# Kernel tuning notes

Measured on AMD Instinct MI355X. Metric: run time of the kernel, lower is better.

Reference implementation:

```python
import jax, jax.numpy as jnp
import numpy as np

BETA = 0.25
TEMP = 1.0
K = 1024          # codebook_size
DIM = 256         # dim == z_dim


def setup_inputs() -> dict:
    key = jax.random.key(0)
    k1, k2, k3 = jax.random.split(key, 3)
    x = jax.random.normal(k1, (8, 4096, DIM), dtype=jnp.float32)
    # Linear: kaiming_uniform -> sqrt(3/fan_in) * U(-1,1); bias init_bias=0 -> zeros
    W = np.sqrt(3.0 / DIM) * (jax.random.uniform(k2, (DIM, DIM), dtype=jnp.float32) * 2 - 1)
    b = jnp.zeros((DIM,), dtype=jnp.float32)
    # embedding: uniform(-1/K, 1/K)
    emb = jax.random.uniform(k3, (K, DIM), dtype=jnp.float32,
                             minval=-1.0 / K, maxval=1.0 / K)
    return {"x": x, "W": W, "b": b, "emb": emb}


def reference(x, W, b, emb):
    # proj_in: x @ W.T + b
    z = jnp.einsum('bld,od->blo', x, W) + b                     # [B, L, D]
    # squared-L2 distances to codebook (use_norm=False branch)
    dist = (jnp.sum(z * z, axis=-1, keepdims=True)
            + jnp.sum(emb * emb, axis=1)
            - 2.0 * jnp.einsum('bld,nd->bln', z, emb))           # [B, L, K]
    indices = jnp.argmin(dist, axis=-1)                          # [B, L] int
    # ste_prob computed in torch forward (affects grads via one_hot, not outputs)
    quant = emb[indices]                                         # [B, L, D]
    # commitment + codebook loss (training=True)
    loss = (BETA * jnp.mean((jax.lax.stop_gradient(quant) - z) ** 2)
            + jnp.mean((quant - jax.lax.stop_gradient(z)) ** 2))
    # straight-through estimator
    quant = z + jax.lax.stop_gradient(quant - z)
    return quant, indices, loss
```

## Files before the change

### kernel.cpp

```cpp
#include <hip/hip_runtime.h>
#include <hip/hip_bf16.h>

#define TT 32768
#define DD 256
#define KK 1024
#define B_S 5e-4f

typedef __attribute__((ext_vector_type(8)))  short bf16x8;
typedef __attribute__((ext_vector_type(4)))  short bf16x4s;
typedef __attribute__((ext_vector_type(16))) float f32x16;

static inline __device__ short f2bf(float v) {
    __hip_bfloat16 h = __float2bfloat16(v);
    return __builtin_bit_cast(short, h);
}
static inline __device__ float bf2f(short s) {
    __hip_bfloat16 h = __builtin_bit_cast(__hip_bfloat16, s);
    return __bfloat162float(h);
}

__global__ void k_ee(const float* __restrict__ emb, float* __restrict__ ee,
                     int* __restrict__ g_nf) {
    if (blockIdx.x == 0 && threadIdx.x == 0) g_nf[0] = 0;
    int n = blockIdx.x * 256 + threadIdx.x;
    if (n >= KK) return;
    const float4* r = (const float4*)(emb + (size_t)n * DD);
    float s = 0.f;
#pragma unroll
    for (int i = 0; i < DD / 4; ++i) {
        float4 v = r[i];
        s += v.x * v.x + v.y * v.y + v.z * v.z + v.w * v.w;
    }
    ee[n] = s;
}

__global__ void k_pack(const float* __restrict__ emb, short* __restrict__ pemb,
                       float4* __restrict__ embP4) {
    int u = blockIdx.x * 256 + threadIdx.x;
    int lane = u & 63;
    int ks  = (u >> 6) & 1, nb = (u >> 7) & 3;
    int kbi = (u >> 9) & 7, nc = (u >> 12) & 7;
    int n = nc * 128 + nb * 32 + (lane & 31);
    int k = kbi * 32 + ks * 16 + (lane >> 5) * 8;
    const float* src = emb + (size_t)n * DD + k;
    float4 v0 = *(const float4*)(src);
    float4 v1 = *(const float4*)(src + 4);
    bf16x8 hb = { f2bf(v0.x), f2bf(v0.y), f2bf(v0.z), f2bf(v0.w),
                  f2bf(v1.x), f2bf(v1.y), f2bf(v1.z), f2bf(v1.w) };
    *(bf16x8*)(pemb + (size_t)u * 8) = hb;
    embP4[(size_t)(k >> 2) * KK + n]       = v0;
    embP4[(size_t)((k >> 2) + 1) * KK + n] = v1;
}

#define PW 40

__launch_bounds__(256, 2)
__global__ void k_proj(const float* __restrict__ x, const float* __restrict__ W,
                       const float* __restrict__ bias, float* __restrict__ z) {
    __shared__ __align__(16) short Ax[3][64 * PW];
    __shared__ __align__(16) short Bw[3][256 * PW];
    const int tid = threadIdx.x;
    const int w = tid >> 6, lane = tid & 63;
    const int l31 = lane & 31, h = lane >> 5;
    const int t0 = blockIdx.x * 64;
    const int wt = (w & 1) * 32;
    const int wc = (w >> 1) * 128;

    f32x16 acc[4];
#pragma unroll
    for (int cb = 0; cb < 4; ++cb)
#pragma unroll
        for (int r = 0; r < 16; ++r) acc[cb][r] = 0.f;

    for (int kb = 0; kb < DD; kb += 32) {
        __syncthreads();
#pragma unroll
        for (int j = 0; j < 2; ++j) {
            int idx = j * 256 + tid, row = idx >> 3, c4 = idx & 7;
            float4 v = *(const float4*)(x + (size_t)(t0 + row) * DD + kb + c4 * 4);
            float e[4] = {v.x, v.y, v.z, v.w};
            bf16x4s s1, s2, s3;
#pragma unroll
            for (int q = 0; q < 4; ++q) {
                short h1 = f2bf(e[q]); float r1 = e[q] - bf2f(h1);
                short h2 = f2bf(r1);   float r2 = r1 - bf2f(h2);
                short h3 = f2bf(r2);
                s1[q] = h1; s2[q] = h2; s3[q] = h3;
            }
            int a = row * PW + c4 * 4;
            *(bf16x4s*)&Ax[0][a] = s1; *(bf16x4s*)&Ax[1][a] = s2; *(bf16x4s*)&Ax[2][a] = s3;
        }
#pragma unroll
        for (int j = 0; j < 8; ++j) {
            int idx = j * 256 + tid, row = idx >> 3, c4 = idx & 7;
            float4 v = *(const float4*)(W + (size_t)row * DD + kb + c4 * 4);
            float e[4] = {v.x, v.y, v.z, v.w};
            bf16x4s s1, s2, s3;
#pragma unroll
            for (int q = 0; q < 4; ++q) {
                short h1 = f2bf(e[q]); float r1 = e[q] - bf2f(h1);
                short h2 = f2bf(r1);   float r2 = r1 - bf2f(h2);
                short h3 = f2bf(r2);
                s1[q] = h1; s2[q] = h2; s3[q] = h3;
            }
            int a = row * PW + c4 * 4;
            *(bf16x4s*)&Bw[0][a] = s1; *(bf16x4s*)&Bw[1][a] = s2; *(bf16x4s*)&Bw[2][a] = s3;
        }
        __syncthreads();
#pragma unroll
        for (int ks = 0; ks < 2; ++ks) {
            int ao = (wt + l31) * PW + ks * 16 + h * 8;
            bf16x8 a1 = *(bf16x8*)&Ax[0][ao];
            bf16x8 a2 = *(bf16x8*)&Ax[1][ao];
            bf16x8 a3 = *(bf16x8*)&Ax[2][ao];
#pragma unroll
            for (int cb = 0; cb < 4; ++cb) {
                int bo = (wc + cb * 32 + l31) * PW + ks * 16 + h * 8;
                bf16x8 b1 = *(bf16x8*)&Bw[0][bo];
                bf16x8 b2 = *(bf16x8*)&Bw[1][bo];
                bf16x8 b3 = *(bf16x8*)&Bw[2][bo];
                acc[cb] = __builtin_amdgcn_mfma_f32_32x32x16_bf16(a1, b3, acc[cb], 0, 0, 0);
                acc[cb] = __builtin_amdgcn_mfma_f32_32x32x16_bf16(a2, b2, acc[cb], 0, 0, 0);
                acc[cb] = __builtin_amdgcn_mfma_f32_32x32x16_bf16(a3, b1, acc[cb], 0, 0, 0);
                acc[cb] = __builtin_amdgcn_mfma_f32_32x32x16_bf16(a1, b2, acc[cb], 0, 0, 0);
                acc[cb] = __builtin_amdgcn_mfma_f32_32x32x16_bf16(a2, b1, acc[cb], 0, 0, 0);
                acc[cb] = __builtin_amdgcn_mfma_f32_32x32x16_bf16(a1, b1, acc[cb], 0, 0, 0);
            }
        }
    }
#pragma unroll
    for (int cb = 0; cb < 4; ++cb) {
        int col = wc + cb * 32 + l31;
        float bc = bias[col];
#pragma unroll
        for (int r = 0; r < 16; ++r) {
            int row = (r & 3) + 8 * (r >> 2) + 4 * h;
            z[(size_t)(t0 + wt + row) * DD + col] = acc[cb][r] + bc;
        }
    }
}

#define SW 264

__launch_bounds__(256, 2)
__global__ void k_screen(const float* __restrict__ z, const short* __restrict__ pemb,
                         const float* __restrict__ ee_g, float* __restrict__ out_idx) {
    __shared__ __align__(16) short A_s[64 * SW];
    __shared__ float ee_s[1024];
    __shared__ float zzs[64];
    __shared__ float r_bv[64]; __shared__ int r_bi[64]; __shared__ float r_sv[64];

    const int tid = threadIdx.x;
    const int w = tid >> 6, lane = tid & 63;
    const int l31 = lane & 31, h = lane >> 5;
    const int t0 = blockIdx.x * 64;
    const int wr = (w >> 1) * 32, wc = (w & 1) * 64;

#pragma unroll
    for (int i = 0; i < 4; ++i) ee_s[i * 256 + tid] = ee_g[i * 256 + tid];

#pragma unroll
    for (int i = 0; i < 16; ++i) {
        int tl = i * 4 + w;
        float4 v = *(const float4*)(z + (size_t)(t0 + tl) * DD + lane * 4);
        float sq = v.x * v.x + v.y * v.y + v.z * v.z + v.w * v.w;
#pragma unroll
        for (int o = 32; o; o >>= 1) sq += __shfl_xor(sq, o);
        if (lane == 0) zzs[tl] = sq;
        bf16x4s hb = {f2bf(v.x), f2bf(v.y), f2bf(v.z), f2bf(v.w)};
        *(bf16x4s*)&A_s[tl * SW + lane * 4] = hb;
    }
    __syncthreads();

    const int u00 = ((((w & 1) * 2 + 0) * 2 + 0) * 64 + lane) * 8;
    const int u01 = ((((w & 1) * 2 + 0) * 2 + 1) * 64 + lane) * 8;
    const int u10 = ((((w & 1) * 2 + 1) * 2 + 0) * 64 + lane) * 8;
    const int u11 = ((((w & 1) * 2 + 1) * 2 + 1) * 64 + lane) * 8;

    bf16x8 B00[4], B01[4], B10[4], B11[4];
#pragma unroll
    for (int s = 0; s < 4; ++s) {
        const short* gt = pemb + (size_t)s * 4096;
        B00[s] = *(const bf16x8*)(gt + u00);
        B01[s] = *(const bf16x8*)(gt + u01);
        B10[s] = *(const bf16x8*)(gt + u10);
        B11[s] = *(const bf16x8*)(gt + u11);
    }

    float bestv[16], secv[16]; int besti[16];
#pragma unroll
    for (int r = 0; r < 16; ++r) { bestv[r] = 1e30f; secv[r] = 1e30f; besti[r] = 0; }

    f32x16 acc0, acc1;
    for (int tq = 0; tq < 16; ++tq) {
#pragma unroll
        for (int s = 0; s < 4; ++s) {
            const int t = tq * 4 + s;
            const int nc = t >> 3, kbi = t & 7;
            if (kbi == 0) {
#pragma unroll
                for (int r = 0; r < 16; ++r) { acc0[r] = 0.f; acc1[r] = 0.f; }
            }
            bf16x8 a0 = *(bf16x8*)&A_s[(wr + l31) * SW + kbi * 32 + 0 * 16 + h * 8];
            bf16x8 a1 = *(bf16x8*)&A_s[(wr + l31) * SW + kbi * 32 + 1 * 16 + h * 8];
            acc0 = __builtin_amdgcn_mfma_f32_32x32x16_bf16(a0, B00[s], acc0, 0, 0, 0);
            acc1 = __builtin_amdgcn_mfma_f32_32x32x16_bf16(a0, B10[s], acc1, 0, 0, 0);
            acc0 = __builtin_amdgcn_mfma_f32_32x32x16_bf16(a1, B01[s], acc0, 0, 0, 0);
            acc1 = __builtin_amdgcn_mfma_f32_32x32x16_bf16(a1, B11[s], acc1, 0, 0, 0);
            {
                const int tn = (t + 4 > 63) ? 63 : t + 4;
                const short* gt = pemb + (size_t)tn * 4096;
                B00[s] = *(const bf16x8*)(gt + u00);
                B01[s] = *(const bf16x8*)(gt + u01);
                B10[s] = *(const bf16x8*)(gt + u10);
                B11[s] = *(const bf16x8*)(gt + u11);
            }
            if (kbi == 7) {
#pragma unroll
                for (int j = 0; j < 2; ++j) {
                    int n = nc * 128 + wc + j * 32 + l31;
                    float en = ee_s[n];
#pragma unroll
                    for (int r = 0; r < 16; ++r) {
                        int row = (r & 3) + 8 * (r >> 2) + 4 * h;
                        float u = zzs[wr + row] + en;
                        float d = (j == 0) ? acc0[r] : acc1[r];
                        float sc = fmaf(-2.f, d, u);
                        if (sc < bestv[r])      { secv[r] = bestv[r]; bestv[r] = sc; besti[r] = n; }
                        else if (sc < secv[r])  { secv[r] = sc; }
                    }
                }
            }
        }
    }

#pragma unroll
    for (int o = 1; o < 32; o <<= 1) {
#pragma unroll
        for (int r = 0; r < 16; ++r) {
            float ov = __shfl_xor(bestv[r], o);
            int   oi = __shfl_xor(besti[r], o);
            float os = __shfl_xor(secv[r], o);
            float mx = fmaxf(bestv[r], ov);
            secv[r] = fminf(fminf(secv[r], os), mx);
            if (ov < bestv[r] || (ov == bestv[r] && oi < besti[r])) { bestv[r] = ov; besti[r] = oi; }
        }
    }
    if ((w & 1) == 0 && l31 == 0) {
#pragma unroll
        for (int r = 0; r < 16; ++r) {
            int tr = wr + (r & 3) + 8 * (r >> 2) + 4 * h;
            r_bv[tr] = bestv[r]; r_bi[tr] = besti[r]; r_sv[tr] = secv[r];
        }
    }
    __syncthreads();
    if ((w & 1) == 1 && l31 == 0) {
#pragma unroll
        for (int r = 0; r < 16; ++r) {
            int tr = wr + (r & 3) + 8 * (r >> 2) + 4 * h;
            float lv = r_bv[tr]; int li = r_bi[tr]; float ls = r_sv[tr];
            float mx = fmaxf(lv, bestv[r]);
            float ns = fminf(fminf(ls, secv[r]), mx);
            float nv; int ni;
            if (bestv[r] < lv || (bestv[r] == lv && besti[r] < li)) { nv = bestv[r]; ni = besti[r]; }
            else { nv = lv; ni = li; }
            r_bv[tr] = nv; r_bi[tr] = ni; r_sv[tr] = ns;
        }
    }
    __syncthreads();
    if (tid < 64) {
        float bv = r_bv[tid], sv = r_sv[tid];
        int bi = r_bi[tid];
        float flag = ((sv - bv) < B_S) ? 4096.0f : 0.0f;
        out_idx[t0 + tid] = (float)bi + flag;
    }
}

__global__ void k_compact(const float* __restrict__ out_idx, int* __restrict__ g_nf,
                          int* __restrict__ g_list) {
    __shared__ int wbase[4];
    __shared__ int bbase;
    const int tid = threadIdx.x;
    const int t = blockIdx.x * 256 + tid;
    const int wid = tid >> 6, lane = tid & 63;
    bool fl = out_idx[t] >= 4096.0f;
    unsigned long long m = __ballot(fl);
    if (lane == 0) wbase[wid] = __popcll(m);
    __syncthreads();
    if (tid == 0) {
        int s = 0;
#pragma unroll
        for (int i = 0; i < 4; ++i) { int c = wbase[i]; wbase[i] = s; s += c; }
        bbase = atomicAdd(g_nf, s);
    }
    __syncthreads();
    if (fl) {
        int rank = __popcll(m & ((1ull << lane) - 1ull));
        g_list[bbase + wbase[wid] + rank] = t;
    }
}

#define RB 8

__launch_bounds__(256, 2)
__global__ void k_rescoreT(const float* __restrict__ z, const float4* __restrict__ embP4,
                           const float* __restrict__ ee_g, const int* __restrict__ g_nf,
                           const int* __restrict__ g_list, float* __restrict__ out_idx) {
    __shared__ float zrows[RB][256];
    __shared__ float zz8[RB];
    __shared__ int   toks[RB];
    __shared__ float rv_s[RB][4]; __shared__ int ri_s[RB][4];
    const int tid = threadIdx.x;
    const int w = tid >> 6, lane = tid & 63;
    const int nf = g_nf[0];

    for (int base = blockIdx.x * RB; base < nf; base += gridDim.x * RB) {
        __syncthreads();
        if (tid < RB) toks[tid] = (base + tid < nf) ? g_list[base + tid] : -1;
        __syncthreads();
#pragma unroll
        for (int qq = 0; qq < RB; ++qq) {
            int tok = toks[qq];
            zrows[qq][tid] = (tok >= 0) ? z[(size_t)tok * DD + tid] : 0.f;
        }
        __syncthreads();
        for (int qq = w; qq < RB; qq += 4) {
            float s = 0.f;
#pragma unroll
            for (int k = 0; k < 4; ++k) { float vv = zrows[qq][lane + 64 * k]; s += vv * vv; }
#pragma unroll
            for (int o = 32; o; o >>= 1) s += __shfl_xor(s, o);
            if (lane == 0) zz8[qq] = s;
        }
        __syncthreads();

        float en4[4];
#pragma unroll
        for (int p = 0; p < 4; ++p) en4[p] = ee_g[p * 256 + tid];

        float d[4][RB];
#pragma unroll
        for (int p = 0; p < 4; ++p)
#pragma unroll
            for (int q = 0; q < RB; ++q) d[p][q] = 0.f;

        float4 eA[4], eB[4], zA[RB], zB[RB];
#pragma unroll
        for (int p = 0; p < 4; ++p) eA[p] = embP4[(size_t)0 * KK + p * 256 + tid];
#pragma unroll
        for (int q = 0; q < RB; ++q) zA[q] = *(const float4*)&zrows[q][0];

        for (int k4 = 0; k4 < 64; k4 += 2) {
#pragma unroll
            for (int p = 0; p < 4; ++p) eB[p] = embP4[(size_t)(k4 + 1) * KK + p * 256 + tid];
#pragma unroll
            for (int q = 0; q < RB; ++q) zB[q] = *(const float4*)&zrows[q][(k4 + 1) * 4];
#pragma unroll
            for (int p = 0; p < 4; ++p)
#pragma unroll
                for (int q = 0; q < RB; ++q) {
                    d[p][q] = fmaf(eA[p].x, zA[q].x, d[p][q]);
                    d[p][q] = fmaf(eA[p].y, zA[q].y, d[p][q]);
                    d[p][q] = fmaf(eA[p].z, zA[q].z, d[p][q]);
                    d[p][q] = fmaf(eA[p].w, zA[q].w, d[p][q]);
                }
            if (k4 < 62) {
#pragma unroll
                for (int p = 0; p < 4; ++p) eA[p] = embP4[(size_t)(k4 + 2) * KK + p * 256 + tid];
#pragma unroll
                for (int q = 0; q < RB; ++q) zA[q] = *(const float4*)&zrows[q][(k4 + 2) * 4];
            }
#pragma unroll
            for (int p = 0; p < 4; ++p)
#pragma unroll
                for (int q = 0; q < RB; ++q) {
                    d[p][q] = fmaf(eB[p].x, zB[q].x, d[p][q]);
                    d[p][q] = fmaf(eB[p].y, zB[q].y, d[p][q]);
                    d[p][q] = fmaf(eB[p].z, zB[q].z, d[p][q]);
                    d[p][q] = fmaf(eB[p].w, zB[q].w, d[p][q]);
                }
        }

        float bv[RB]; int bi[RB];
#pragma unroll
        for (int q = 0; q < RB; ++q) { bv[q] = 1e30f; bi[q] = 0; }
#pragma unroll
        for (int p = 0; p < 4; ++p) {
            const int n = p * 256 + tid;
#pragma unroll
            for (int q = 0; q < RB; ++q) {
                float u = zz8[q] + en4[p];
                float s = fmaf(-2.f, d[p][q], u);
                if (s < bv[q]) { bv[q] = s; bi[q] = n; }
            }
        }
        for (int q = 0; q < RB; ++q) {
            float v = bv[q]; int i = bi[q];
#pragma unroll
            for (int o = 1; o < 64; o <<= 1) {
                float ov = __shfl_xor(v, o); int oi = __shfl_xor(i, o);
                if (ov < v || (ov == v && oi < i)) { v = ov; i = oi; }
            }
            if (lane == 0) { rv_s[q][w] = v; ri_s[q][w] = i; }
        }
        __syncthreads();
        if (tid < RB) {
            int tk = toks[tid];
            if (tk >= 0) {
                float fv = rv_s[tid][0]; int fi = ri_s[tid][0];
#pragma unroll
                for (int ww = 1; ww < 4; ++ww) {
                    if (rv_s[tid][ww] < fv || (rv_s[tid][ww] == fv && ri_s[tid][ww] < fi)) {
                        fv = rv_s[tid][ww]; fi = ri_s[tid][ww];
                    }
                }
                out_idx[tk] = (float)fi;
            }
        }
    }
}

__global__ void k_gather(float* __restrict__ zq, const float* __restrict__ emb,
                         const float* __restrict__ out_idx, float* __restrict__ partial) {
    __shared__ float red[4];
    const int tid = threadIdx.x;
    const int t0 = blockIdx.x * 128;
    const int tl = tid >> 1, part = tid & 1;
    int widx = (int)out_idx[t0 + tl];
    widx = min(max(widx, 0), KK - 1);
    const float* erow = emb + (size_t)widx * DD;
    float* qrow = zq + (size_t)(t0 + tl) * DD;
    float lsum = 0.f;
#pragma unroll
    for (int k = 0; k < 32; ++k) {
        int f = part + 2 * k;
        float4 e  = *(const float4*)(erow + f * 4);
        float4 zv = *(const float4*)(qrow + f * 4);
        float dx = e.x - zv.x, dy = e.y - zv.y, dz = e.z - zv.z, dw = e.w - zv.w;
        lsum += dx * dx + dy * dy + dz * dz + dw * dw;
        *(float4*)(qrow + f * 4) = e;
    }
#pragma unroll
    for (int off = 32; off; off >>= 1) lsum += __shfl_down(lsum, off);
    if ((tid & 63) == 0) red[tid >> 6] = lsum;
    __syncthreads();
    if (tid == 0) partial[blockIdx.x] = red[0] + red[1] + red[2] + red[3];
}

__global__ void k_loss(const float* __restrict__ partial, float* __restrict__ out_loss) {
    __shared__ float red[4];
    int tid = threadIdx.x;
    float s = partial[tid];
#pragma unroll
    for (int off = 32; off; off >>= 1) s += __shfl_down(s, off);
    if ((tid & 63) == 0) red[tid >> 6] = s;
    __syncthreads();
    if (tid == 0)
        out_loss[0] = (red[0] + red[1] + red[2] + red[3]) * (1.25f / 8388608.0f);
}

extern "C" void kernel_launch(void* const* d_in, const int* in_sizes, int n_in,
                              void* d_out, int out_size, void* d_ws, size_t ws_size,
                              hipStream_t stream) {
    const float* x   = (const float*)d_in[0];
    const float* W   = (const float*)d_in[1];
    const float* b   = (const float*)d_in[2];
    const float* emb = (const float*)d_in[3];

    float* out   = (float*)d_out;
    float* quant = out;
    float* oidx  = out + (size_t)TT * DD;
    float* oloss = oidx + TT;

    float* wsf     = (float*)d_ws;
    float* ee      = wsf;
    float* partial = wsf + 1024;
    short* pemb    = (short*)(wsf + 1280);
    int*   g_nf    = (int*)(wsf + 132352);
    int*   g_list  = (int*)(wsf + 132353);
    float4* embP4  = (float4*)(wsf + 165124);

    k_ee      <<<KK / 256, 256, 0, stream>>>(emb, ee, g_nf);
    k_pack    <<<128,      256, 0, stream>>>(emb, pemb, embP4);
    k_proj    <<<TT / 64,  256, 0, stream>>>(x, W, b, quant);
    k_screen  <<<TT / 64,  256, 0, stream>>>(quant, pemb, ee, oidx);
    k_compact <<<TT / 256, 256, 0, stream>>>(oidx, g_nf, g_list);
    k_rescoreT<<<512,      256, 0, stream>>>(quant, embP4, ee, g_nf, g_list, oidx);
    k_gather  <<<TT / 128, 256, 0, stream>>>(quant, emb, oidx, partial);
    k_loss    <<<1,        256, 0, stream>>>(partial, oloss);
}
```

Measured before the change: 270.9 us.

## Stage codebook tiles into LDS via async global_load_lds double buffering

The screening kernel now keeps the whole A tile (z rows in bf16) in registers and streams packed codebook tiles into a 64 KB double-buffered LDS region with global_load_lds. Previously each wave loaded B fragments straight from global memory into registers. Each phase covers 64 codes, with one accumulator per wave and a 32-column slice per wave. This is meant to cut redundant global traffic and register pressure from B prefetching, but it adds LDS pressure that may limit occupancy, plus a barrier per phase.

```diff
diff --git a/kernel.cpp b/kernel.cpp
--- a/kernel.cpp
+++ b/kernel.cpp
@@ -17,6 +17,13 @@
 static inline __device__ float bf2f(short s) {
     __hip_bfloat16 h = __builtin_bit_cast(__hip_bfloat16, s);
     return __bfloat162float(h);
+}
+
+static inline __device__ void gload16(const void* g, void* l) {
+    __builtin_amdgcn_global_load_lds(
+        (const __attribute__((address_space(1))) void*)g,
+        (__attribute__((address_space(3))) void*)l,
+        16, 0, 0);
 }
 
 __global__ void k_ee(const float* __restrict__ emb, float* __restrict__ ee,
@@ -145,16 +152,18 @@
 __launch_bounds__(256, 2)
 __global__ void k_screen(const float* __restrict__ z, const short* __restrict__ pemb,
                          const float* __restrict__ ee_g, float* __restrict__ out_idx) {
-    __shared__ __align__(16) short A_s[64 * SW];
+    __shared__ __align__(16) char smem[65536];
     __shared__ float ee_s[1024];
     __shared__ float zzs[64];
     __shared__ float r_bv[64]; __shared__ int r_bi[64]; __shared__ float r_sv[64];
 
+    short* A_s = (short*)smem;
     const int tid = threadIdx.x;
     const int w = tid >> 6, lane = tid & 63;
     const int l31 = lane & 31, h = lane >> 5;
     const int t0 = blockIdx.x * 64;
-    const int wr = (w >> 1) * 32, wc = (w & 1) * 64;
+    const int wr = (w >> 1) * 32;
+    const int hw = w & 1;
 
 #pragma unroll
     for (int i = 0; i < 4; ++i) ee_s[i * 256 + tid] = ee_g[i * 256 + tid];
@@ -172,64 +181,56 @@
     }
     __syncthreads();
 
-    const int u00 = ((((w & 1) * 2 + 0) * 2 + 0) * 64 + lane) * 8;
-    const int u01 = ((((w & 1) * 2 + 0) * 2 + 1) * 64 + lane) * 8;
-    const int u10 = ((((w & 1) * 2 + 1) * 2 + 0) * 64 + lane) * 8;
-    const int u11 = ((((w & 1) * 2 + 1) * 2 + 1) * 64 + lane) * 8;
-
-    bf16x8 B00[4], B01[4], B10[4], B11[4];
-#pragma unroll
-    for (int s = 0; s < 4; ++s) {
-        const short* gt = pemb + (size_t)s * 4096;
-        B00[s] = *(const bf16x8*)(gt + u00);
-        B01[s] = *(const bf16x8*)(gt + u01);
-        B10[s] = *(const bf16x8*)(gt + u10);
-        B11[s] = *(const bf16x8*)(gt + u11);
-    }
+    bf16x8 af[16];
+#pragma unroll
+    for (int kbi = 0; kbi < 8; ++kbi)
+#pragma unroll
+        for (int ks = 0; ks < 2; ++ks)
+            af[kbi * 2 + ks] = *(bf16x8*)&A_s[(wr + l31) * SW + kbi * 32 + ks * 16 + h * 8];
+    __syncthreads();
+
+    const char* pB = (const char*)pemb;
+#pragma unroll
+    for (int j = 0; j < 8; ++j)
+        gload16(pB + j * 8192 + w * 1024 + lane * 16, smem + j * 4096 + w * 1024);
 
     float bestv[16], secv[16]; int besti[16];
 #pragma unroll
     for (int r = 0; r < 16; ++r) { bestv[r] = 1e30f; secv[r] = 1e30f; besti[r] = 0; }
 
-    f32x16 acc0, acc1;
-    for (int tq = 0; tq < 16; ++tq) {
-#pragma unroll
-        for (int s = 0; s < 4; ++s) {
-            const int t = tq * 4 + s;
-            const int nc = t >> 3, kbi = t & 7;
-            if (kbi == 0) {
-#pragma unroll
-                for (int r = 0; r < 16; ++r) { acc0[r] = 0.f; acc1[r] = 0.f; }
-            }
-            bf16x8 a0 = *(bf16x8*)&A_s[(wr + l31) * SW + kbi * 32 + 0 * 16 + h * 8];
-            bf16x8 a1 = *(bf16x8*)&A_s[(wr + l31) * SW + kbi * 32 + 1 * 16 + h * 8];
-            acc0 = __builtin_amdgcn_mfma_f32_32x32x16_bf16(a0, B00[s], acc0, 0, 0, 0);
-            acc1 = __builtin_amdgcn_mfma_f32_32x32x16_bf16(a0, B10[s], acc1, 0, 0, 0);
-            acc0 = __builtin_amdgcn_mfma_f32_32x32x16_bf16(a1, B01[s], acc0, 0, 0, 0);
-            acc1 = __builtin_amdgcn_mfma_f32_32x32x16_bf16(a1, B11[s], acc1, 0, 0, 0);
-            {
-                const int tn = (t + 4 > 63) ? 63 : t + 4;
-                const short* gt = pemb + (size_t)tn * 4096;
-                B00[s] = *(const bf16x8*)(gt + u00);
-                B01[s] = *(const bf16x8*)(gt + u01);
-                B10[s] = *(const bf16x8*)(gt + u10);
-                B11[s] = *(const bf16x8*)(gt + u11);
-            }
-            if (kbi == 7) {
-#pragma unroll
-                for (int j = 0; j < 2; ++j) {
-                    int n = nc * 128 + wc + j * 32 + l31;
-                    float en = ee_s[n];
-#pragma unroll
-                    for (int r = 0; r < 16; ++r) {
-                        int row = (r & 3) + 8 * (r >> 2) + 4 * h;
-                        float u = zzs[wr + row] + en;
-                        float d = (j == 0) ? acc0[r] : acc1[r];
-                        float sc = fmaf(-2.f, d, u);
-                        if (sc < bestv[r])      { secv[r] = bestv[r]; bestv[r] = sc; besti[r] = n; }
-                        else if (sc < secv[r])  { secv[r] = sc; }
-                    }
-                }
+    for (int ph = 0; ph < 16; ++ph) {
+        const int buf = ph & 1;
+        char* Bb = smem + buf * 32768;
+        asm volatile("s_waitcnt vmcnt(0)" ::: "memory");
+        __syncthreads();
+        if (ph < 15) {
+            const int nn = ph + 1;
+            const char* src = pB + (size_t)(nn >> 1) * 65536 + (nn & 1) * 4096;
+            char* dst = smem + (buf ^ 1) * 32768;
+#pragma unroll
+            for (int j = 0; j < 8; ++j)
+                gload16(src + j * 8192 + w * 1024 + lane * 16, dst + j * 4096 + w * 1024);
+        }
+        f32x16 acc;
+#pragma unroll
+        for (int r = 0; r < 16; ++r) acc[r] = 0.f;
+#pragma unroll
+        for (int kbi = 0; kbi < 8; ++kbi) {
+            bf16x8 b0 = *(bf16x8*)(Bb + kbi * 4096 + (hw * 2 + 0) * 1024 + lane * 16);
+            bf16x8 b1 = *(bf16x8*)(Bb + kbi * 4096 + (hw * 2 + 1) * 1024 + lane * 16);
+            acc = __builtin_amdgcn_mfma_f32_32x32x16_bf16(af[kbi * 2 + 0], b0, acc, 0, 0, 0);
+            acc = __builtin_amdgcn_mfma_f32_32x32x16_bf16(af[kbi * 2 + 1], b1, acc, 0, 0, 0);
+        }
+        {
+            int n = (ph >> 1) * 128 + (ph & 1) * 64 + hw * 32 + l31;
+            float en = ee_s[n];
+#pragma unroll
+            for (int r = 0; r < 16; ++r) {
+                int row = (r & 3) + 8 * (r >> 2) + 4 * h;
+                float u = zzs[wr + row] + en;
+                float sc = fmaf(-2.f, acc[r], u);
+                if (sc < bestv[r])      { secv[r] = bestv[r]; bestv[r] = sc; besti[r] = n; }
+                else if (sc < secv[r])  { secv[r] = sc; }
             }
         }
     }
```

Result: no change. 275.0 us (+1.5%).
